# Kernel tuning notes

Measured on AMD Instinct MI355X. Metric: run time of the kernel, lower is better.

The kernel has to match this reference:

```python
import jax, jax.numpy as jnp
import numpy as np

N_NODES = 50000
N_EDGES = 800000
IN_DIM = 96
HID_DIM = 96


def setup_inputs() -> dict:
    key = jax.random.key(0)
    ks = jax.random.split(key, 8)
    inputs = jax.random.normal(ks[0], (N_NODES, IN_DIM), dtype=jnp.float32)
    factor = jax.random.uniform(ks[1], (N_EDGES, 1), dtype=jnp.float32)
    src = jax.random.randint(ks[2], (N_EDGES,), 0, N_NODES, dtype=jnp.int32)
    dst = jax.random.randint(ks[3], (N_EDGES,), 0, N_NODES, dtype=jnp.int32)
    # Linear params (torch nn.Linear: y = x @ W.T + b), uniform(-1/sqrt(fan_in), ..)
    s1 = 1.0 / np.sqrt(IN_DIM)
    s2 = 1.0 / np.sqrt(HID_DIM)
    W1 = jax.random.uniform(ks[4], (HID_DIM, IN_DIM), minval=-s1, maxval=s1, dtype=jnp.float32)
    b1 = jax.random.uniform(ks[5], (HID_DIM,), minval=-s1, maxval=s1, dtype=jnp.float32)
    W2 = jax.random.uniform(ks[6], (IN_DIM, HID_DIM), minval=-s2, maxval=s2, dtype=jnp.float32)
    b2 = jax.random.uniform(ks[7], (IN_DIM,), minval=-s2, maxval=s2, dtype=jnp.float32)
    return {"inputs": inputs, "W1": W1, "b1": b1, "W2": W2, "b2": b2,
            "factor": factor, "src": src, "dst": dst}


def _propagate(feat, factor, src, dst, n_nodes):
    # message = h[src] * edge_factor ; reduce = sum at dst
    msg = feat[src] * factor                       # [E, D]
    return jax.ops.segment_sum(msg, dst, num_segments=n_nodes)


def reference(inputs, W1, b1, W2, b2, factor, src, dst):
    n = inputs.shape[0]
    # in-degree norm: deg^{-1/2}, clamped at 1
    deg = jax.ops.segment_sum(jnp.ones((src.shape[0],), inputs.dtype), dst,
                              num_segments=n)
    norm = jnp.maximum(deg, 1.0) ** -0.5           # [N]
    norm = norm[:, None]                           # [N, 1]

    feat = (inputs @ W1.T + b1) * norm             # [N, H]
    h = jnp.tanh(_propagate(feat, factor, src, dst, n))

    feat = (h @ W2.T + b2) * norm                  # [N, D]
    h = jnp.tanh(_propagate(feat, factor, src, dst, n))

    # dgl.mean_nodes over a single graph -> [1, D]; unsqueeze(-1) -> [1, D, 1]
    pooled = jnp.mean(h, axis=0, keepdims=True)[..., None]
    return jnp.tanh(pooled)
```

## Files before the change

### kernel.cpp

```cpp
#include <hip/hip_runtime.h>
#include <math.h>
#include <type_traits>

#define N_NODES 50000
#define N_EDGES 800000
#define DIM 96
#define BCH 12
#define SCAN_BLK 256
#define NBLK ((N_NODES + SCAN_BLK - 1) / SCAN_BLK)
#define NPB 21
#define NBG ((N_NODES + NPB - 1) / NPB)
#define CAP 768
#define R1_ROWS 24
#define R1_BLOCKS ((NBG + R1_ROWS - 1) / R1_ROWS)
#define SC_PASSES 4
#define SC_WIN ((N_NODES + SC_PASSES - 1) / SC_PASSES)

typedef short v8s __attribute__((ext_vector_type(8)));
typedef float v4f __attribute__((ext_vector_type(4)));

__device__ __forceinline__ unsigned short f2bf(float f) {
    unsigned int u = __float_as_uint(f);
    u += 0x7FFFu + ((u >> 16) & 1u);
    return (unsigned short)(u >> 16);
}
__device__ __forceinline__ unsigned int pack2bf(float lo, float hi) {
    return (unsigned int)f2bf(lo) | ((unsigned int)f2bf(hi) << 16);
}
__device__ __forceinline__ float bflo(unsigned int u) { return __uint_as_float(u << 16); }
__device__ __forceinline__ float bfhi(unsigned int u) { return __uint_as_float(u & 0xFFFF0000u); }

__device__ __forceinline__ float fast_tanh(float x) {
    float ax = fabsf(x);
    float t = __expf(-2.0f * ax);
    float r = (1.0f - t) / (1.0f + t);
    return copysignf(r, x);
}

__device__ __forceinline__ void acc8(float* a, uint4 v, float f) {
    a[0] += bflo(v.x) * f; a[1] += bfhi(v.x) * f;
    a[2] += bflo(v.y) * f; a[3] += bfhi(v.y) * f;
    a[4] += bflo(v.z) * f; a[5] += bfhi(v.z) * f;
    a[6] += bflo(v.w) * f; a[7] += bfhi(v.w) * f;
}

union U4S8 { uint4 u; v8s s; };


__global__ void count_deg(const int* __restrict__ dst, int* __restrict__ deg,
                          int* __restrict__ rank) {
    int e = blockIdx.x * blockDim.x + threadIdx.x;
    if (e < N_EDGES) rank[e] = atomicAdd(&deg[dst[e]], 1);
}

__global__ void deg_partials(const int* __restrict__ deg, float* __restrict__ norm,
                             int* __restrict__ partials) {
    int b = blockIdx.x, t = threadIdx.x;
    int n = b * SCAN_BLK + t;
    int v = 0;
    if (n < N_NODES) {
        v = deg[n];
        norm[n] = rsqrtf(fmaxf((float)v, 1.0f));
    }
    int s = v;
#pragma unroll
    for (int off = 32; off > 0; off >>= 1) s += __shfl_down(s, off, 64);
    __shared__ int ws_[4];
    if ((t & 63) == 0) ws_[t >> 6] = s;
    __syncthreads();
    if (t == 0) partials[b] = ws_[0] + ws_[1] + ws_[2] + ws_[3];
}

__global__ void scan_partials(const int* __restrict__ partials, int* __restrict__ pprefix) {
    __shared__ int sm[SCAN_BLK];
    int t = threadIdx.x;
    int v = (t < NBLK) ? partials[t] : 0;
    sm[t] = v;
    __syncthreads();
    for (int off = 1; off < SCAN_BLK; off <<= 1) {
        int u = (t >= off) ? sm[t - off] : 0;
        __syncthreads();
        sm[t] += u;
        __syncthreads();
    }
    if (t < NBLK) pprefix[t] = sm[t] - v;
}

__global__ void make_offsets(const int* __restrict__ deg, const int* __restrict__ pprefix,
                             int* __restrict__ offs) {
    __shared__ int sm[SCAN_BLK];
    int b = blockIdx.x, t = threadIdx.x;
    int idx = b * SCAN_BLK + t;
    int v = (idx < N_NODES) ? deg[idx] : 0;
    sm[t] = v;
    __syncthreads();
    for (int off = 1; off < SCAN_BLK; off <<= 1) {
        int u = (t >= off) ? sm[t - off] : 0;
        __syncthreads();
        sm[t] += u;
        __syncthreads();
    }
    if (idx < N_NODES) offs[idx] = pprefix[b] + sm[t] - v;
    if (b == 0 && t == 0) offs[N_NODES] = N_EDGES;
}

__global__ void scatter_edges(const int* __restrict__ src, const int* __restrict__ dst,
                              const float* __restrict__ factor, const int* __restrict__ rank,
                              const int* __restrict__ offs, int2* __restrict__ entries) {
    int tid0 = blockIdx.x * blockDim.x + threadIdx.x;
    int stride = gridDim.x * blockDim.x;
#pragma unroll 1
    for (int pass = 0; pass < SC_PASSES; ++pass) {
        int lo = pass * SC_WIN;
        int hi = min(lo + SC_WIN, N_NODES);
#pragma unroll 1
        for (int e = tid0; e < N_EDGES; e += stride) {
            int d = dst[e];
            if (d >= lo && d < hi) {
                int pos = offs[d] + rank[e];
                entries[pos] = make_int2(src[e], __float_as_int(factor[e]));
            }
        }
    }
}


__global__ void swizzle_W(const float* __restrict__ W, uint4* __restrict__ bsw) {
    int idx = blockIdx.x * blockDim.x + threadIdx.x;
    if (idx >= 18 * 64) return;
    int t = idx >> 6, lane = idx & 63;
    int kt = t / 6, jt = t % 6;
    int quad = lane >> 4, l16 = lane & 15;
    const float4* wp = (const float4*)(W + (size_t)(jt * 16 + l16) * DIM + kt * 32 + quad * 8);
    float4 w0 = wp[0], w1 = wp[1];
    bsw[idx] = make_uint4(pack2bf(w0.x, w0.y), pack2bf(w0.z, w0.w),
                          pack2bf(w1.x, w1.y), pack2bf(w1.z, w1.w));
}


#define TILE_SH 104

template <typename T>
__global__ __launch_bounds__(256) void gemm_mfma(const T* __restrict__ X,
                                                 const uint4* __restrict__ bsw,
                                                 const float* __restrict__ bias,
                                                 const float* __restrict__ norm,
                                                 unsigned short* __restrict__ out) {
    __shared__ unsigned short tile[4][16 * TILE_SH];
    int tid = threadIdx.x;
    int wave = tid >> 6, lane = tid & 63;
    int quad = lane >> 4, l16 = lane & 15;
    int n0 = blockIdx.x * 64 + wave * 16;
    int rowc = min(n0 + l16, N_NODES - 1);

    uint4 bfr[18];
#pragma unroll
    for (int t = 0; t < 18; ++t) bfr[t] = bsw[t * 64 + lane];

    v4f acc[6];
#pragma unroll
    for (int jt = 0; jt < 6; ++jt) acc[jt] = (v4f)(0.0f);

#pragma unroll
    for (int kt = 0; kt < 3; ++kt) {
        U4S8 a;
        if constexpr (std::is_same_v<T, float>) {
            const float4* xp = (const float4*)(X + (size_t)rowc * DIM + kt * 32 + quad * 8);
            float4 x0 = xp[0], x1 = xp[1];
            a.u = make_uint4(pack2bf(x0.x, x0.y), pack2bf(x0.z, x0.w),
                             pack2bf(x1.x, x1.y), pack2bf(x1.z, x1.w));
        } else {
            a.u = *(const uint4*)(X + (size_t)rowc * DIM + kt * 32 + quad * 8);
        }
#pragma unroll
        for (int jt = 0; jt < 6; ++jt) {
            U4S8 bb; bb.u = bfr[kt * 6 + jt];
            acc[jt] = __builtin_amdgcn_mfma_f32_16x16x32_bf16(a.s, bb.s, acc[jt], 0, 0, 0);
        }
    }

    float nm[4];
#pragma unroll
    for (int r = 0; r < 4; ++r) nm[r] = norm[min(n0 + quad * 4 + r, N_NODES - 1)];
#pragma unroll
    for (int jt = 0; jt < 6; ++jt) {
        float bj = bias[jt * 16 + l16];
#pragma unroll
        for (int r = 0; r < 4; ++r) {
            float v = (acc[jt][r] + bj) * nm[r];
            tile[wave][(quad * 4 + r) * TILE_SH + jt * 16 + l16] = f2bf(v);
        }
    }
    __builtin_amdgcn_s_waitcnt(0);
#pragma unroll
    for (int i = 0; i < 3; ++i) {
        int chunk = lane + 64 * i;
        int rr = chunk / 12, cc = chunk - rr * 12;
        int gn = n0 + rr;
        if (gn < N_NODES) {
            uint4 v = *(uint4*)&tile[wave][rr * TILE_SH + cc * 8];
            *(uint4*)(out + (size_t)gn * DIM + cc * 8) = v;
        }
    }
}


template <bool DO_TANH, bool POOL>
__global__ void gather_agg_bf16(const unsigned short* __restrict__ feat,
                                const int* __restrict__ offs,
                                const int2* __restrict__ entries,
                                unsigned short* __restrict__ out,
                                float* __restrict__ partials) {
    __shared__ int2 ents[CAP];
    __shared__ float pool[DIM];
    __shared__ int sh_base, sh_cnt;
    int tid = threadIdx.x;
    int n0 = blockIdx.x * NPB;
    int n1 = min(n0 + NPB, N_NODES);
    if (POOL && tid < DIM) pool[tid] = 0.f;
    if (tid == 0) { sh_base = offs[n0]; sh_cnt = offs[n1] - sh_base; }
    __syncthreads();
    int base = sh_base, cnt = sh_cnt;

    int nl = tid / BCH;
    int c  = tid - nl * BCH;
    int n  = n0 + nl;
    bool active = (tid < NPB * BCH) && (n < N_NODES);
    int lb = 0, le = 0;
    if (active) { lb = offs[n] - base; le = offs[n + 1] - base; }

    float a0[8], a1[8];
#pragma unroll
    for (int i = 0; i < 8; ++i) { a0[i] = 0.f; a1[i] = 0.f; }

    for (int tb = 0; tb < cnt; tb += CAP) {
        int tcnt = min(cnt - tb, CAP);
        if (tb) __syncthreads();
        for (int i = tid; i < tcnt; i += 256) ents[i] = entries[base + tb + i];
        __syncthreads();
        int s = max(lb - tb, 0), e = min(le - tb, tcnt);
        int p = s;
        for (; p + 7 < e; p += 8) {
            int2 q0 = ents[p + 0], q1 = ents[p + 1], q2 = ents[p + 2], q3 = ents[p + 3];
            int2 q4 = ents[p + 4], q5 = ents[p + 5], q6 = ents[p + 6], q7 = ents[p + 7];
            uint4 v0 = *((const uint4*)(feat + (size_t)q0.x * DIM) + c);
            uint4 v1 = *((const uint4*)(feat + (size_t)q1.x * DIM) + c);
            uint4 v2 = *((const uint4*)(feat + (size_t)q2.x * DIM) + c);
            uint4 v3 = *((const uint4*)(feat + (size_t)q3.x * DIM) + c);
            uint4 v4 = *((const uint4*)(feat + (size_t)q4.x * DIM) + c);
            uint4 v5 = *((const uint4*)(feat + (size_t)q5.x * DIM) + c);
            uint4 v6 = *((const uint4*)(feat + (size_t)q6.x * DIM) + c);
            uint4 v7 = *((const uint4*)(feat + (size_t)q7.x * DIM) + c);
            acc8(a0, v0, __int_as_float(q0.y));
            acc8(a1, v1, __int_as_float(q1.y));
            acc8(a0, v2, __int_as_float(q2.y));
            acc8(a1, v3, __int_as_float(q3.y));
            acc8(a0, v4, __int_as_float(q4.y));
            acc8(a1, v5, __int_as_float(q5.y));
            acc8(a0, v6, __int_as_float(q6.y));
            acc8(a1, v7, __int_as_float(q7.y));
        }
        for (; p + 3 < e; p += 4) {
            int2 q0 = ents[p], q1 = ents[p + 1], q2 = ents[p + 2], q3 = ents[p + 3];
            uint4 v0 = *((const uint4*)(feat + (size_t)q0.x * DIM) + c);
            uint4 v1 = *((const uint4*)(feat + (size_t)q1.x * DIM) + c);
            uint4 v2 = *((const uint4*)(feat + (size_t)q2.x * DIM) + c);
            uint4 v3 = *((const uint4*)(feat + (size_t)q3.x * DIM) + c);
            acc8(a0, v0, __int_as_float(q0.y));
            acc8(a1, v1, __int_as_float(q1.y));
            acc8(a0, v2, __int_as_float(q2.y));
            acc8(a1, v3, __int_as_float(q3.y));
        }
        for (; p < e; ++p) {
            int2 q0 = ents[p];
            uint4 v0 = *((const uint4*)(feat + (size_t)q0.x * DIM) + c);
            acc8(a0, v0, __int_as_float(q0.y));
        }
    }

#pragma unroll
    for (int i = 0; i < 8; ++i) a0[i] += a1[i];
    if (DO_TANH || POOL) {
#pragma unroll
        for (int i = 0; i < 8; ++i) a0[i] = fast_tanh(a0[i]);
    }
    if (!POOL) {
        if (active) {
            uint4 o;
            o.x = pack2bf(a0[0], a0[1]);
            o.y = pack2bf(a0[2], a0[3]);
            o.z = pack2bf(a0[4], a0[5]);
            o.w = pack2bf(a0[6], a0[7]);
            ((uint4*)out)[n * BCH + c] = o;
        }
    } else {
        if (active) {
#pragma unroll
            for (int i = 0; i < 8; ++i) atomicAdd(&pool[c * 8 + i], a0[i]);
        }
        __syncthreads();
        if (tid < DIM) partials[(size_t)blockIdx.x * DIM + tid] = pool[tid];
    }
}


__global__ void reduce_stage1(const float* __restrict__ poolpart, float* __restrict__ stage1) {
    __shared__ float pool[DIM];
    int b = blockIdx.x, t = threadIdx.x;
    if (t < DIM) pool[t] = 0.f;
    __syncthreads();
    const int base = b * R1_ROWS * DIM;
    float loc = 0.f;
    int lastc = -1;
    for (int i = t; i < R1_ROWS * DIM; i += 256) {
        int gi = base + i;
        if (gi < NBG * DIM) {
            int col = i % DIM;
            if (col != lastc) {
                if (lastc >= 0) atomicAdd(&pool[lastc], loc);
                lastc = col; loc = 0.f;
            }
            loc += poolpart[gi];
        }
    }
    if (lastc >= 0) atomicAdd(&pool[lastc], loc);
    __syncthreads();
    if (t < DIM) stage1[b * DIM + t] = pool[t];
}

__global__ void reduce_stage2(const float* __restrict__ stage1, float* __restrict__ out) {
    __shared__ float sm[960];
    int t = threadIdx.x;
    int col = t % DIM, slice = t / DIM;
    float s = 0.f;
    for (int k = slice; k < R1_BLOCKS; k += 10) s += stage1[k * DIM + col];
    sm[t] = s;
    __syncthreads();
    if (t < DIM) {
        float tot = 0.f;
#pragma unroll
        for (int i = 0; i < 10; ++i) tot += sm[i * DIM + t];
        out[t] = tanhf(tot * (1.0f / N_NODES));
    }
}


extern "C" void kernel_launch(void* const* d_in, const int* in_sizes, int n_in,
                              void* d_out, int out_size, void* d_ws, size_t ws_size,
                              hipStream_t stream) {
    const float* inputs = (const float*)d_in[0];
    const float* W1     = (const float*)d_in[1];
    const float* b1     = (const float*)d_in[2];
    const float* W2     = (const float*)d_in[3];
    const float* b2     = (const float*)d_in[4];
    const float* factor = (const float*)d_in[5];
    const int*   src    = (const int*)d_in[6];
    const int*   dst    = (const int*)d_in[7];
    float* out = (float*)d_out;

    char* ws = (char*)d_ws;
    int*            deg      = (int*)(ws + 0);
    int*            rank     = (int*)(ws + 262144);
    int*            offs     = (int*)(ws + 3932160);
    float*          norm     = (float*)(ws + 4194304);
    int*            partials = (int*)(ws + 4456448);
    int*            pprefix  = (int*)(ws + 4458496);
    int2*           entries  = (int2*)(ws + 4718592);
    unsigned short* bufA     = (unsigned short*)(ws + 11534336);
    unsigned short* bufB     = (unsigned short*)(ws + 21364736);
    float*          poolpart = (float*)(ws + 31195136);
    float*          stage1   = (float*)(ws + 32145536);
    uint4*          bsw1     = (uint4*)(ws + 33554432);
    uint4*          bsw2     = (uint4*)(ws + 33574912);

    swizzle_W<<<5, 256, 0, stream>>>(W1, bsw1);
    swizzle_W<<<5, 256, 0, stream>>>(W2, bsw2);

    hipMemsetAsync(deg, 0, N_NODES * sizeof(int), stream);
    count_deg<<<(N_EDGES + 255) / 256, 256, 0, stream>>>(dst, deg, rank);
    deg_partials<<<NBLK, SCAN_BLK, 0, stream>>>(deg, norm, partials);
    scan_partials<<<1, SCAN_BLK, 0, stream>>>(partials, pprefix);
    make_offsets<<<NBLK, SCAN_BLK, 0, stream>>>(deg, pprefix, offs);
    scatter_edges<<<2048, 256, 0, stream>>>(src, dst, factor, rank, offs, entries);

    const int GEMM_BLOCKS = (N_NODES + 63) / 64;

    gemm_mfma<float><<<GEMM_BLOCKS, 256, 0, stream>>>(inputs, bsw1, b1, norm, bufA);
    gather_agg_bf16<true, false><<<NBG, 256, 0, stream>>>(bufA, offs, entries, bufB, nullptr);

    gemm_mfma<unsigned short><<<GEMM_BLOCKS, 256, 0, stream>>>(bufB, bsw2, b2, norm, bufA);
    gather_agg_bf16<false, true><<<NBG, 256, 0, stream>>>(bufA, offs, entries, nullptr, poolpart);

    reduce_stage1<<<R1_BLOCKS, 256, 0, stream>>>(poolpart, stage1);
    reduce_stage2<<<1, 960, 0, stream>>>(stage1, out);
}
```

Baseline: 237.3 us.

## Bin CSR edges by source range within each destination for gather locality

Counts edges per (destination, source-bin) pair and scans these bins, so each destination's edge list is ordered by coarse source index. The goal is more localized feature-row reads during the two gather-aggregate passes. It costs a larger count array to memset, a 16-entry per-node scan, and extra offset writes in preprocessing.

```diff
diff --git a/kernel.cpp b/kernel.cpp
--- a/kernel.cpp
+++ b/kernel.cpp
@@ -15,6 +15,7 @@
 #define R1_BLOCKS ((NBG + R1_ROWS - 1) / R1_ROWS)
 #define SC_PASSES 4
 #define SC_WIN ((N_NODES + SC_PASSES - 1) / SC_PASSES)
+#define NBIN 16
 
 typedef short v8s __attribute__((ext_vector_type(8)));
 typedef float v4f __attribute__((ext_vector_type(4)));
@@ -47,26 +48,36 @@
 union U4S8 { uint4 u; v8s s; };
 
 
-__global__ void count_deg(const int* __restrict__ dst, int* __restrict__ deg,
-                          int* __restrict__ rank) {
+__global__ void count_bins(const int* __restrict__ src, const int* __restrict__ dst,
+                           int* __restrict__ cnt, int* __restrict__ rank) {
     int e = blockIdx.x * blockDim.x + threadIdx.x;
-    if (e < N_EDGES) rank[e] = atomicAdd(&deg[dst[e]], 1);
-}
-
-__global__ void deg_partials(const int* __restrict__ deg, float* __restrict__ norm,
-                             int* __restrict__ partials) {
+    if (e >= N_EDGES) return;
+    int d = dst[e];
+    int b = src[e] >> 12;
+    rank[e] = atomicAdd(&cnt[d * NBIN + b], 1);
+}
+
+__global__ void node_pass(int* __restrict__ cnt, int* __restrict__ deg,
+                          float* __restrict__ norm, int* __restrict__ partials) {
     int b = blockIdx.x, t = threadIdx.x;
     int n = b * SCAN_BLK + t;
-    int v = 0;
+    int s = 0;
     if (n < N_NODES) {
-        v = deg[n];
-        norm[n] = rsqrtf(fmaxf((float)v, 1.0f));
-    }
-    int s = v;
-#pragma unroll
-    for (int off = 32; off > 0; off >>= 1) s += __shfl_down(s, off, 64);
+        int base = n * NBIN;
+#pragma unroll
+        for (int k = 0; k < NBIN; ++k) {
+            int c = cnt[base + k];
+            cnt[base + k] = s;
+            s += c;
+        }
+        deg[n] = s;
+        norm[n] = rsqrtf(fmaxf((float)s, 1.0f));
+    }
+    int v = s;
+#pragma unroll
+    for (int off = 32; off > 0; off >>= 1) v += __shfl_down(v, off, 64);
     __shared__ int ws_[4];
-    if ((t & 63) == 0) ws_[t >> 6] = s;
+    if ((t & 63) == 0) ws_[t >> 6] = v;
     __syncthreads();
     if (t == 0) partials[b] = ws_[0] + ws_[1] + ws_[2] + ws_[3];
 }
@@ -87,7 +98,8 @@
 }
 
 __global__ void make_offsets(const int* __restrict__ deg, const int* __restrict__ pprefix,
-                             int* __restrict__ offs) {
+                             const int* __restrict__ cnt, int* __restrict__ offs,
+                             int* __restrict__ offs2) {
     __shared__ int sm[SCAN_BLK];
     int b = blockIdx.x, t = threadIdx.x;
     int idx = b * SCAN_BLK + t;
@@ -100,13 +112,19 @@
         sm[t] += u;
         __syncthreads();
     }
-    if (idx < N_NODES) offs[idx] = pprefix[b] + sm[t] - v;
+    if (idx < N_NODES) {
+        int o = pprefix[b] + sm[t] - v;
+        offs[idx] = o;
+        int base = idx * NBIN;
+#pragma unroll
+        for (int k = 0; k < NBIN; ++k) offs2[base + k] = o + cnt[base + k];
+    }
     if (b == 0 && t == 0) offs[N_NODES] = N_EDGES;
 }
 
 __global__ void scatter_edges(const int* __restrict__ src, const int* __restrict__ dst,
                               const float* __restrict__ factor, const int* __restrict__ rank,
-                              const int* __restrict__ offs, int2* __restrict__ entries) {
+                              const int* __restrict__ offs2, int2* __restrict__ entries) {
     int tid0 = blockIdx.x * blockDim.x + threadIdx.x;
     int stride = gridDim.x * blockDim.x;
 #pragma unroll 1
@@ -117,8 +135,9 @@
         for (int e = tid0; e < N_EDGES; e += stride) {
             int d = dst[e];
             if (d >= lo && d < hi) {
-                int pos = offs[d] + rank[e];
-                entries[pos] = make_int2(src[e], __float_as_int(factor[e]));
+                int s = src[e];
+                int pos = offs2[d * NBIN + (s >> 12)] + rank[e];
+                entries[pos] = make_int2(s, __float_as_int(factor[e]));
             }
         }
     }
@@ -372,16 +391,18 @@
     float*          stage1   = (float*)(ws + 32145536);
     uint4*          bsw1     = (uint4*)(ws + 33554432);
     uint4*          bsw2     = (uint4*)(ws + 33574912);
+    int*            cnt      = (int*)(ws + 11534336);
+    int*            offs2    = (int*)(ws + 14942208);
 
     swizzle_W<<<5, 256, 0, stream>>>(W1, bsw1);
     swizzle_W<<<5, 256, 0, stream>>>(W2, bsw2);
 
-    hipMemsetAsync(deg, 0, N_NODES * sizeof(int), stream);
-    count_deg<<<(N_EDGES + 255) / 256, 256, 0, stream>>>(dst, deg, rank);
-    deg_partials<<<NBLK, SCAN_BLK, 0, stream>>>(deg, norm, partials);
+    hipMemsetAsync(cnt, 0, N_NODES * NBIN * sizeof(int), stream);
+    count_bins<<<(N_EDGES + 255) / 256, 256, 0, stream>>>(src, dst, cnt, rank);
+    node_pass<<<NBLK, SCAN_BLK, 0, stream>>>(cnt, deg, norm, partials);
     scan_partials<<<1, SCAN_BLK, 0, stream>>>(partials, pprefix);
-    make_offsets<<<NBLK, SCAN_BLK, 0, stream>>>(deg, pprefix, offs);
-    scatter_edges<<<2048, 256, 0, stream>>>(src, dst, factor, rank, offs, entries);
+    make_offsets<<<NBLK, SCAN_BLK, 0, stream>>>(deg, pprefix, cnt, offs, offs2);
+    scatter_edges<<<2048, 256, 0, stream>>>(src, dst, factor, rank, offs2, entries);
 
     const int GEMM_BLOCKS = (N_NODES + 63) / 64;
 
```

Result: slower. 242.8 us (+2.3%).

## Store projected node features as scaled FP8 to halve gather traffic

Applied to the files above, without the earlier changes.

The GEMM epilogue now writes node features as FP8 (scaled by 16) rather than bf16. It swaps the MFMA operand order so each lane holds four consecutive columns of one node and can store them directly, which removes the shared-memory staging tile. The gather kernels load 8-byte FP8 chunks per lane instead of 16-byte bf16 chunks, decode them with the packed fp8-to-f32 conversion, and unscale before tanh. This roughly halves the bytes fetched by the random-access gathers, at the cost of FP8 precision loss in the intermediate features.

```diff
diff --git a/kernel.cpp b/kernel.cpp
--- a/kernel.cpp
+++ b/kernel.cpp
@@ -15,9 +15,12 @@
 #define R1_BLOCKS ((NBG + R1_ROWS - 1) / R1_ROWS)
 #define SC_PASSES 4
 #define SC_WIN ((N_NODES + SC_PASSES - 1) / SC_PASSES)
+#define F8_SCALE 16.0f
+#define F8_INV   0.0625f
 
 typedef short v8s __attribute__((ext_vector_type(8)));
 typedef float v4f __attribute__((ext_vector_type(4)));
+typedef float v2f __attribute__((ext_vector_type(2)));
 
 __device__ __forceinline__ unsigned short f2bf(float f) {
     unsigned int u = __float_as_uint(f);
@@ -27,8 +30,6 @@
 __device__ __forceinline__ unsigned int pack2bf(float lo, float hi) {
     return (unsigned int)f2bf(lo) | ((unsigned int)f2bf(hi) << 16);
 }
-__device__ __forceinline__ float bflo(unsigned int u) { return __uint_as_float(u << 16); }
-__device__ __forceinline__ float bfhi(unsigned int u) { return __uint_as_float(u & 0xFFFF0000u); }
 
 __device__ __forceinline__ float fast_tanh(float x) {
     float ax = fabsf(x);
@@ -37,11 +38,15 @@
     return copysignf(r, x);
 }
 
-__device__ __forceinline__ void acc8(float* a, uint4 v, float f) {
-    a[0] += bflo(v.x) * f; a[1] += bfhi(v.x) * f;
-    a[2] += bflo(v.y) * f; a[3] += bfhi(v.y) * f;
-    a[4] += bflo(v.z) * f; a[5] += bfhi(v.z) * f;
-    a[6] += bflo(v.w) * f; a[7] += bfhi(v.w) * f;
+__device__ __forceinline__ void accf8(float* a, uint2 v, float f) {
+    v2f p0 = __builtin_amdgcn_cvt_pk_f32_fp8(v.x, false);
+    v2f p1 = __builtin_amdgcn_cvt_pk_f32_fp8(v.x, true);
+    v2f p2 = __builtin_amdgcn_cvt_pk_f32_fp8(v.y, false);
+    v2f p3 = __builtin_amdgcn_cvt_pk_f32_fp8(v.y, true);
+    a[0] += p0.x * f; a[1] += p0.y * f;
+    a[2] += p1.x * f; a[3] += p1.y * f;
+    a[4] += p2.x * f; a[5] += p2.y * f;
+    a[6] += p3.x * f; a[7] += p3.y * f;
 }
 
 union U4S8 { uint4 u; v8s s; };
@@ -138,20 +143,18 @@
 }
 
 
-#define TILE_SH 104
-
 template <typename T>
 __global__ __launch_bounds__(256) void gemm_mfma(const T* __restrict__ X,
                                                  const uint4* __restrict__ bsw,
                                                  const float* __restrict__ bias,
                                                  const float* __restrict__ norm,
-                                                 unsigned short* __restrict__ out) {
-    __shared__ unsigned short tile[4][16 * TILE_SH];
+                                                 unsigned char* __restrict__ out) {
     int tid = threadIdx.x;
     int wave = tid >> 6, lane = tid & 63;
     int quad = lane >> 4, l16 = lane & 15;
     int n0 = blockIdx.x * 64 + wave * 16;
-    int rowc = min(n0 + l16, N_NODES - 1);
+    int node = n0 + l16;
+    int rowc = min(node, N_NODES - 1);
 
     uint4 bfr[18];
 #pragma unroll
@@ -163,54 +166,45 @@
 
 #pragma unroll
     for (int kt = 0; kt < 3; ++kt) {
-        U4S8 a;
+        U4S8 x;
         if constexpr (std::is_same_v<T, float>) {
             const float4* xp = (const float4*)(X + (size_t)rowc * DIM + kt * 32 + quad * 8);
             float4 x0 = xp[0], x1 = xp[1];
-            a.u = make_uint4(pack2bf(x0.x, x0.y), pack2bf(x0.z, x0.w),
+            x.u = make_uint4(pack2bf(x0.x, x0.y), pack2bf(x0.z, x0.w),
                              pack2bf(x1.x, x1.y), pack2bf(x1.z, x1.w));
         } else {
-            a.u = *(const uint4*)(X + (size_t)rowc * DIM + kt * 32 + quad * 8);
+            x.u = *(const uint4*)(X + (size_t)rowc * DIM + kt * 32 + quad * 8);
         }
 #pragma unroll
         for (int jt = 0; jt < 6; ++jt) {
-            U4S8 bb; bb.u = bfr[kt * 6 + jt];
-            acc[jt] = __builtin_amdgcn_mfma_f32_16x16x32_bf16(a.s, bb.s, acc[jt], 0, 0, 0);
-        }
-    }
-
-    float nm[4];
-#pragma unroll
-    for (int r = 0; r < 4; ++r) nm[r] = norm[min(n0 + quad * 4 + r, N_NODES - 1)];
-#pragma unroll
-    for (int jt = 0; jt < 6; ++jt) {
-        float bj = bias[jt * 16 + l16];
-#pragma unroll
-        for (int r = 0; r < 4; ++r) {
-            float v = (acc[jt][r] + bj) * nm[r];
-            tile[wave][(quad * 4 + r) * TILE_SH + jt * 16 + l16] = f2bf(v);
-        }
-    }
-    __builtin_amdgcn_s_waitcnt(0);
-#pragma unroll
-    for (int i = 0; i < 3; ++i) {
-        int chunk = lane + 64 * i;
-        int rr = chunk / 12, cc = chunk - rr * 12;
-        int gn = n0 + rr;
-        if (gn < N_NODES) {
-            uint4 v = *(uint4*)&tile[wave][rr * TILE_SH + cc * 8];
-            *(uint4*)(out + (size_t)gn * DIM + cc * 8) = v;
-        }
-    }
-}
-
-
-template <bool DO_TANH, bool POOL>
-__global__ void gather_agg_bf16(const unsigned short* __restrict__ feat,
-                                const int* __restrict__ offs,
-                                const int2* __restrict__ entries,
-                                unsigned short* __restrict__ out,
-                                float* __restrict__ partials) {
+            U4S8 w; w.u = bfr[kt * 6 + jt];
+            acc[jt] = __builtin_amdgcn_mfma_f32_16x16x32_bf16(w.s, x.s, acc[jt], 0, 0, 0);
+        }
+    }
+
+    if (node < N_NODES) {
+        float nm = norm[node] * F8_SCALE;
+#pragma unroll
+        for (int jt = 0; jt < 6; ++jt) {
+            float4 bj = *(const float4*)(bias + jt * 16 + quad * 4);
+            float v0 = (acc[jt][0] + bj.x) * nm;
+            float v1 = (acc[jt][1] + bj.y) * nm;
+            float v2 = (acc[jt][2] + bj.z) * nm;
+            float v3 = (acc[jt][3] + bj.w) * nm;
+            unsigned int w = (unsigned int)__builtin_amdgcn_cvt_pk_fp8_f32(v0, v1, 0, false);
+            w = (unsigned int)__builtin_amdgcn_cvt_pk_fp8_f32(v2, v3, (int)w, true);
+            *(unsigned int*)(out + (size_t)node * DIM + jt * 16 + quad * 4) = w;
+        }
+    }
+}
+
+
+template <bool POOL>
+__global__ void gather_agg_f8(const unsigned char* __restrict__ feat,
+                              const int* __restrict__ offs,
+                              const int2* __restrict__ entries,
+                              unsigned short* __restrict__ out,
+                              float* __restrict__ partials) {
     __shared__ int2 ents[CAP];
     __shared__ float pool[DIM];
     __shared__ int sh_base, sh_cnt;
@@ -243,47 +237,43 @@
         for (; p + 7 < e; p += 8) {
             int2 q0 = ents[p + 0], q1 = ents[p + 1], q2 = ents[p + 2], q3 = ents[p + 3];
             int2 q4 = ents[p + 4], q5 = ents[p + 5], q6 = ents[p + 6], q7 = ents[p + 7];
-            uint4 v0 = *((const uint4*)(feat + (size_t)q0.x * DIM) + c);
-            uint4 v1 = *((const uint4*)(feat + (size_t)q1.x * DIM) + c);
-            uint4 v2 = *((const uint4*)(feat + (size_t)q2.x * DIM) + c);
-            uint4 v3 = *((const uint4*)(feat + (size_t)q3.x * DIM) + c);
-            uint4 v4 = *((const uint4*)(feat + (size_t)q4.x * DIM) + c);
-            uint4 v5 = *((const uint4*)(feat + (size_t)q5.x * DIM) + c);
-            uint4 v6 = *((const uint4*)(feat + (size_t)q6.x * DIM) + c);
-            uint4 v7 = *((const uint4*)(feat + (size_t)q7.x * DIM) + c);
-            acc8(a0, v0, __int_as_float(q0.y));
-            acc8(a1, v1, __int_as_float(q1.y));
-            acc8(a0, v2, __int_as_float(q2.y));
-            acc8(a1, v3, __int_as_float(q3.y));
-            acc8(a0, v4, __int_as_float(q4.y));
-            acc8(a1, v5, __int_as_float(q5.y));
-            acc8(a0, v6, __int_as_float(q6.y));
-            acc8(a1, v7, __int_as_float(q7.y));
+            uint2 v0 = *((const uint2*)(feat + (size_t)q0.x * DIM) + c);
+            uint2 v1 = *((const uint2*)(feat + (size_t)q1.x * DIM) + c);
+            uint2 v2 = *((const uint2*)(feat + (size_t)q2.x * DIM) + c);
+            uint2 v3 = *((const uint2*)(feat + (size_t)q3.x * DIM) + c);
+            uint2 v4 = *((const uint2*)(feat + (size_t)q4.x * DIM) + c);
+            uint2 v5 = *((const uint2*)(feat + (size_t)q5.x * DIM) + c);
+            uint2 v6 = *((const uint2*)(feat + (size_t)q6.x * DIM) + c);
+            uint2 v7 = *((const uint2*)(feat + (size_t)q7.x * DIM) + c);
+            accf8(a0, v0, __int_as_float(q0.y));
+            accf8(a1, v1, __int_as_float(q1.y));
+            accf8(a0, v2, __int_as_float(q2.y));
+            accf8(a1, v3, __int_as_float(q3.y));
+            accf8(a0, v4, __int_as_float(q4.y));
+            accf8(a1, v5, __int_as_float(q5.y));
+            accf8(a0, v6, __int_as_float(q6.y));
+            accf8(a1, v7, __int_as_float(q7.y));
         }
         for (; p + 3 < e; p += 4) {
             int2 q0 = ents[p], q1 = ents[p + 1], q2 = ents[p + 2], q3 = ents[p + 3];
-            uint4 v0 = *((const uint4*)(feat + (size_t)q0.x * DIM) + c);
-            uint4 v1 = *((const uint4*)(feat + (size_t)q1.x * DIM) + c);
-            uint4 v2 = *((const uint4*)(feat + (size_t)q2.x * DIM) + c);
-            uint4 v3 = *((const uint4*)(feat + (size_t)q3.x * DIM) + c);
-            acc8(a0, v0, __int_as_float(q0.y));
-            acc8(a1, v1, __int_as_float(q1.y));
-            acc8(a0, v2, __int_as_float(q2.y));
-            acc8(a1, v3, __int_as_float(q3.y));
+            uint2 v0 = *((const uint2*)(feat + (size_t)q0.x * DIM) + c);
+            uint2 v1 = *((const uint2*)(feat + (size_t)q1.x * DIM) + c);
+            uint2 v2 = *((const uint2*)(feat + (size_t)q2.x * DIM) + c);
+            uint2 v3 = *((const uint2*)(feat + (size_t)q3.x * DIM) + c);
+            accf8(a0, v0, __int_as_float(q0.y));
+            accf8(a1, v1, __int_as_float(q1.y));
+            accf8(a0, v2, __int_as_float(q2.y));
+            accf8(a1, v3, __int_as_float(q3.y));
         }
         for (; p < e; ++p) {
             int2 q0 = ents[p];
-            uint4 v0 = *((const uint4*)(feat + (size_t)q0.x * DIM) + c);
-            acc8(a0, v0, __int_as_float(q0.y));
-        }
-    }
-
-#pragma unroll
-    for (int i = 0; i < 8; ++i) a0[i] += a1[i];
-    if (DO_TANH || POOL) {
-#pragma unroll
-        for (int i = 0; i < 8; ++i) a0[i] = fast_tanh(a0[i]);
-    }
+            uint2 v0 = *((const uint2*)(feat + (size_t)q0.x * DIM) + c);
+            accf8(a0, v0, __int_as_float(q0.y));
+        }
+    }
+
+#pragma unroll
+    for (int i = 0; i < 8; ++i) a0[i] = fast_tanh((a0[i] + a1[i]) * F8_INV);
     if (!POOL) {
         if (active) {
             uint4 o;
@@ -366,7 +356,7 @@
     int*            partials = (int*)(ws + 4456448);
     int*            pprefix  = (int*)(ws + 4458496);
     int2*           entries  = (int2*)(ws + 4718592);
-    unsigned short* bufA     = (unsigned short*)(ws + 11534336);
+    unsigned char*  bufA     = (unsigned char*)(ws + 11534336);
     unsigned short* bufB     = (unsigned short*)(ws + 21364736);
     float*          poolpart = (float*)(ws + 31195136);
     float*          stage1   = (float*)(ws + 32145536);
@@ -386,10 +376,10 @@
     const int GEMM_BLOCKS = (N_NODES + 63) / 64;
 
     gemm_mfma<float><<<GEMM_BLOCKS, 256, 0, stream>>>(inputs, bsw1, b1, norm, bufA);
-    gather_agg_bf16<true, false><<<NBG, 256, 0, stream>>>(bufA, offs, entries, bufB, nullptr);
+    gather_agg_f8<false><<<NBG, 256, 0, stream>>>(bufA, offs, entries, bufB, nullptr);
 
     gemm_mfma<unsigned short><<<GEMM_BLOCKS, 256, 0, stream>>>(bufB, bsw2, b2, norm, bufA);
-    gather_agg_bf16<false, true><<<NBG, 256, 0, stream>>>(bufA, offs, entries, nullptr, poolpart);
+    gather_agg_f8<true><<<NBG, 256, 0, stream>>>(bufA, offs, entries, nullptr, poolpart);
 
     reduce_stage1<<<R1_BLOCKS, 256, 0, stream>>>(poolpart, stage1);
     reduce_stage2<<<1, 960, 0, stream>>>(stage1, out);
```

Result: no change. 232.6 us (-2.0%).
